# Optimization experiments

Measured on AMD Instinct MI355X. Metric: run time of the kernel, lower is better.

## Reference

```python
import jax, jax.numpy as jnp
import numpy as np

N, E, T = 32768, 262144, 262144
DN, DE = 128, 128
EPS = 1e-5  # torch LayerNorm default eps


def layer_norm(x, g, b):
    m = jnp.mean(x, axis=-1, keepdims=True)
    v = jnp.mean((x - m) ** 2, axis=-1, keepdims=True)
    return (x - m) * jax.lax.rsqrt(v + EPS) * g + b


def setup_inputs() -> dict:
    key = jax.random.key(0)
    ks = jax.random.split(key, 16)
    node_embedding = jax.random.normal(ks[0], (N, DN), dtype=jnp.float32)
    edge_embedding = jax.random.normal(ks[1], (E, DE), dtype=jnp.float32)
    i = jax.random.randint(ks[2], (E,), 0, N)
    j = jax.random.randint(ks[3], (E,), 0, N)
    index_i = jax.random.randint(ks[4], (T,), 0, N)
    index_j = jax.random.randint(ks[5], (T,), 0, N)
    index_k = jax.random.randint(ks[6], (T,), 0, N)
    index_ji = jax.random.randint(ks[7], (T,), 0, E)
    index_kj = jax.random.randint(ks[8], (T,), 0, E)
    d3 = 3 * DN + 2 * DE
    W2 = jax.random.normal(ks[9], (2 * DE, DN), dtype=jnp.float32) / np.sqrt(DN)
    b2 = jnp.zeros((2 * DE,), dtype=jnp.float32)
    W3 = jax.random.normal(ks[10], (2 * DE, d3), dtype=jnp.float32) / np.sqrt(d3)
    b3 = jnp.zeros((2 * DE,), dtype=jnp.float32)
    g_c2 = jnp.ones((2 * DE,), jnp.float32); be_c2 = jnp.zeros((2 * DE,), jnp.float32)
    g_c3 = jnp.ones((2 * DE,), jnp.float32); be_c3 = jnp.zeros((2 * DE,), jnp.float32)
    g_c2_2 = jnp.ones((DE,), jnp.float32); be_c2_2 = jnp.zeros((DE,), jnp.float32)
    g_c3_2 = jnp.ones((DE,), jnp.float32); be_c3_2 = jnp.zeros((DE,), jnp.float32)
    return dict(node_embedding=node_embedding, edge_embedding=edge_embedding,
                i=i, j=j, index_i=index_i, index_j=index_j, index_k=index_k,
                index_ji=index_ji, index_kj=index_kj,
                W2=W2, b2=b2, W3=W3, b3=b3,
                g_c2=g_c2, be_c2=be_c2, g_c3=g_c3, be_c3=be_c3,
                g_c2_2=g_c2_2, be_c2_2=be_c2_2, g_c3_2=g_c3_2, be_c3_2=be_c3_2)


def reference(node_embedding, edge_embedding, i, j, index_i, index_j, index_k,
              index_ji, index_kj, W2, b2, W3, b3,
              g_c2, be_c2, g_c3, be_c3, g_c2_2, be_c2_2, g_c3_2, be_c3_2):
    num_edges = edge_embedding.shape[0]
    # --- c2 branch: per-edge elementwise product of endpoint node embeddings ---
    c2 = node_embedding[i] * node_embedding[j]                      # [E, Dn]
    c2 = layer_norm(c2 @ W2.T + b2, g_c2, be_c2)                    # [E, 2De]
    c2_filter, c2_core = jnp.split(c2, 2, axis=1)
    c2_emb = layer_norm(jax.nn.sigmoid(c2_filter) * jnp.tanh(c2_core), g_c2_2, be_c2_2)
    # --- c3 branch: triplet gather -> linear -> LN -> gate -> scatter-sum ---
    c3 = jnp.concatenate([node_embedding[index_i], node_embedding[index_j],
                          node_embedding[index_k], edge_embedding[index_ji],
                          edge_embedding[index_kj]], axis=1)        # [T, 3Dn+2De]
    c3 = layer_norm(c3 @ W3.T + b3, g_c3, be_c3)                    # [T, 2De]
    c3_filter, c3_core = jnp.split(c3, 2, axis=1)
    msg = jax.nn.sigmoid(c3_filter) * jnp.tanh(c3_core)             # [T, De]
    c3_emb = jax.ops.segment_sum(msg, index_ji, num_segments=num_edges)  # [E, De]
    c3_emb = layer_norm(c3_emb, g_c3_2, be_c3_2)
    return jnp.tanh(edge_embedding + c2_emb + c3_emb)
```

## Files before the change

kernel.cpp:

```cpp
#include <hip/hip_runtime.h>

typedef _Float16 h16;
typedef _Float16 h16x8 __attribute__((ext_vector_type(8)));
typedef float    f32x4 __attribute__((ext_vector_type(4)));

static constexpr int NN  = 32768;
static constexpr int EE  = 262144;
static constexpr int TT  = 262144;
static constexpr int D   = 128;
static constexpr int K3  = 640;
static constexpr int LDA = 72;
#define EPS 1e-5f

__global__ __launch_bounds__(256) void cvt_f32_f16(
    const float* __restrict__ src, h16* __restrict__ dst, int n8)
{
    const int i = blockIdx.x * 256 + threadIdx.x;
    if (i >= n8) return;
    const float4* s = reinterpret_cast<const float4*>(src);
    const float4 a = s[2 * i], b = s[2 * i + 1];
    h16x8 o;
    o[0] = (h16)a.x; o[1] = (h16)a.y; o[2] = (h16)a.z; o[3] = (h16)a.w;
    o[4] = (h16)b.x; o[5] = (h16)b.y; o[6] = (h16)b.z; o[7] = (h16)b.w;
    *reinterpret_cast<h16x8*>(dst + 8 * i) = o;
}

__global__ __launch_bounds__(256, 2) void c3_kernel(
    const h16*  __restrict__ nodeh, const float* __restrict__ edge,
    const int* __restrict__ idx_i, const int* __restrict__ idx_j,
    const int* __restrict__ idx_k, const int* __restrict__ idx_ji,
    const int* __restrict__ idx_kj,
    const h16* __restrict__ W3h, const float* __restrict__ b3,
    const float* __restrict__ g3, const float* __restrict__ be3,
    float* __restrict__ acc3)
{
    __shared__ h16 As[128 * LDA];
    __shared__ h16 Bs[256 * LDA];

    const int tid  = threadIdx.x;
    const int lane = tid & 63;
    const int wave = tid >> 6;
    const int l15  = lane & 15;
    const int quad = lane >> 4;
    const int m0   = blockIdx.x * 128;

    f32x4 acc[2][16];
    #pragma unroll
    for (int mt = 0; mt < 2; ++mt)
        #pragma unroll
        for (int nt = 0; nt < 16; ++nt)
            acc[mt][nt] = (f32x4){0.f, 0.f, 0.f, 0.f};

    const int r = tid >> 1;
    const int h = tid & 1;

    #pragma unroll 1
    for (int c = 0; c < 10; ++c) {
        const int seg  = c >> 1;
        const int half = c & 1;
        const int* idxarr = (seg == 0) ? idx_i : (seg == 1) ? idx_j
                          : (seg == 2) ? idx_k : (seg == 3) ? idx_ji : idx_kj;
        const size_t row = (size_t)idxarr[m0 + r];
        h16x8 av[4];
        if (seg < 3) {
            const h16x8* sp = reinterpret_cast<const h16x8*>(nodeh + row * D + half * 64 + h * 32);
            #pragma unroll
            for (int q = 0; q < 4; ++q) av[q] = sp[q];
        } else {
            const float4* fp = reinterpret_cast<const float4*>(edge + row * D + half * 64 + h * 32);
            #pragma unroll
            for (int q = 0; q < 4; ++q) {
                const float4 u = fp[2 * q], v = fp[2 * q + 1];
                h16x8 t;
                t[0] = (h16)u.x; t[1] = (h16)u.y; t[2] = (h16)u.z; t[3] = (h16)u.w;
                t[4] = (h16)v.x; t[5] = (h16)v.y; t[6] = (h16)v.z; t[7] = (h16)v.w;
                av[q] = t;
            }
        }
        const h16x8* wp = reinterpret_cast<const h16x8*>(W3h + (size_t)tid * K3 + c * 64);
        h16x8 bv[8];
        #pragma unroll
        for (int q = 0; q < 8; ++q) bv[q] = wp[q];

        __syncthreads();
        h16x8* ad = reinterpret_cast<h16x8*>(&As[r * LDA + h * 32]);
        #pragma unroll
        for (int q = 0; q < 4; ++q) ad[q] = av[q];
        h16x8* bd = reinterpret_cast<h16x8*>(&Bs[tid * LDA]);
        #pragma unroll
        for (int q = 0; q < 8; ++q) bd[q] = bv[q];
        __syncthreads();

        #pragma unroll
        for (int kk = 0; kk < 64; kk += 32) {
            h16x8 a0 = *reinterpret_cast<const h16x8*>(&As[(wave*32      + l15) * LDA + kk + quad*8]);
            h16x8 a1 = *reinterpret_cast<const h16x8*>(&As[(wave*32 + 16 + l15) * LDA + kk + quad*8]);
            #pragma unroll
            for (int nt = 0; nt < 16; ++nt) {
                h16x8 b = *reinterpret_cast<const h16x8*>(&Bs[(nt*16 + l15) * LDA + kk + quad*8]);
                acc[0][nt] = __builtin_amdgcn_mfma_f32_16x16x32_f16(a0, b, acc[0][nt], 0, 0, 0);
                acc[1][nt] = __builtin_amdgcn_mfma_f32_16x16x32_f16(a1, b, acc[1][nt], 0, 0, 0);
            }
        }
    }

    float bias[16], gg[16], bb[16];
    #pragma unroll
    for (int nt = 0; nt < 16; ++nt) {
        const int cc = nt * 16 + l15;
        bias[nt] = b3[cc]; gg[nt] = g3[cc]; bb[nt] = be3[cc];
    }
    #pragma unroll
    for (int mt = 0; mt < 2; ++mt) {
        #pragma unroll
        for (int rg = 0; rg < 4; ++rg) {
            float v[16];
            float s = 0.f, s2 = 0.f;
            #pragma unroll
            for (int nt = 0; nt < 16; ++nt) {
                v[nt] = acc[mt][nt][rg] + bias[nt];
                s += v[nt]; s2 += v[nt] * v[nt];
            }
            #pragma unroll
            for (int m = 1; m < 16; m <<= 1) {
                s  += __shfl_xor(s,  m, 64);
                s2 += __shfl_xor(s2, m, 64);
            }
            const float mean = s * (1.f / 256.f);
            const float var  = s2 * (1.f / 256.f) - mean * mean;
            const float inv  = rsqrtf(var + EPS);
            const int rowg   = m0 + wave * 32 + mt * 16 + quad * 4 + rg;
            const size_t e   = (size_t)idx_ji[rowg];
            #pragma unroll
            for (int nt = 0; nt < 8; ++nt) {
                const float f   = (v[nt]     - mean) * inv * gg[nt]     + bb[nt];
                const float co  = (v[nt + 8] - mean) * inv * gg[nt + 8] + bb[nt + 8];
                const float msg = (1.f / (1.f + __expf(-f))) * tanhf(co);
                atomicAdd(&acc3[e * D + nt * 16 + l15], msg);
            }
        }
    }
}

__global__ __launch_bounds__(256, 2) void c2_kernel(
    const h16* __restrict__ nodeh,
    const int* __restrict__ ei, const int* __restrict__ ej,
    const h16* __restrict__ W2h, const float* __restrict__ b2,
    const float* __restrict__ g2, const float* __restrict__ be2,
    const float* __restrict__ g22, const float* __restrict__ be22,
    h16* __restrict__ c2emb)
{
    __shared__ h16 As[128 * LDA];
    __shared__ h16 Bs[256 * LDA];

    const int tid  = threadIdx.x;
    const int lane = tid & 63;
    const int wave = tid >> 6;
    const int l15  = lane & 15;
    const int quad = lane >> 4;
    const int m0   = blockIdx.x * 128;

    f32x4 acc[2][16];
    #pragma unroll
    for (int mt = 0; mt < 2; ++mt)
        #pragma unroll
        for (int nt = 0; nt < 16; ++nt)
            acc[mt][nt] = (f32x4){0.f, 0.f, 0.f, 0.f};

    const int r = tid >> 1;
    const int h = tid & 1;
    const size_t ri = (size_t)ei[m0 + r];
    const size_t rj = (size_t)ej[m0 + r];

    #pragma unroll 1
    for (int c = 0; c < 2; ++c) {
        const h16x8* si = reinterpret_cast<const h16x8*>(nodeh + ri * D + c * 64 + h * 32);
        const h16x8* sj = reinterpret_cast<const h16x8*>(nodeh + rj * D + c * 64 + h * 32);
        h16x8 av[4];
        #pragma unroll
        for (int q = 0; q < 4; ++q) av[q] = si[q] * sj[q];
        const h16x8* wp = reinterpret_cast<const h16x8*>(W2h + (size_t)tid * D + c * 64);
        h16x8 bv[8];
        #pragma unroll
        for (int q = 0; q < 8; ++q) bv[q] = wp[q];

        __syncthreads();
        h16x8* ad = reinterpret_cast<h16x8*>(&As[r * LDA + h * 32]);
        #pragma unroll
        for (int q = 0; q < 4; ++q) ad[q] = av[q];
        h16x8* bd = reinterpret_cast<h16x8*>(&Bs[tid * LDA]);
        #pragma unroll
        for (int q = 0; q < 8; ++q) bd[q] = bv[q];
        __syncthreads();

        #pragma unroll
        for (int kk = 0; kk < 64; kk += 32) {
            h16x8 a0 = *reinterpret_cast<const h16x8*>(&As[(wave*32      + l15) * LDA + kk + quad*8]);
            h16x8 a1 = *reinterpret_cast<const h16x8*>(&As[(wave*32 + 16 + l15) * LDA + kk + quad*8]);
            #pragma unroll
            for (int nt = 0; nt < 16; ++nt) {
                h16x8 b = *reinterpret_cast<const h16x8*>(&Bs[(nt*16 + l15) * LDA + kk + quad*8]);
                acc[0][nt] = __builtin_amdgcn_mfma_f32_16x16x32_f16(a0, b, acc[0][nt], 0, 0, 0);
                acc[1][nt] = __builtin_amdgcn_mfma_f32_16x16x32_f16(a1, b, acc[1][nt], 0, 0, 0);
            }
        }
    }

    float bias[16], gg[16], bb[16];
    #pragma unroll
    for (int nt = 0; nt < 16; ++nt) {
        const int cc = nt * 16 + l15;
        bias[nt] = b2[cc]; gg[nt] = g2[cc]; bb[nt] = be2[cc];
    }
    float g2c[8], b2c[8];
    #pragma unroll
    for (int nt = 0; nt < 8; ++nt) {
        const int cc = nt * 16 + l15;
        g2c[nt] = g22[cc]; b2c[nt] = be22[cc];
    }
    #pragma unroll
    for (int mt = 0; mt < 2; ++mt) {
        #pragma unroll
        for (int rg = 0; rg < 4; ++rg) {
            float v[16];
            float s = 0.f, s2 = 0.f;
            #pragma unroll
            for (int nt = 0; nt < 16; ++nt) {
                v[nt] = acc[mt][nt][rg] + bias[nt];
                s += v[nt]; s2 += v[nt] * v[nt];
            }
            #pragma unroll
            for (int m = 1; m < 16; m <<= 1) {
                s  += __shfl_xor(s,  m, 64);
                s2 += __shfl_xor(s2, m, 64);
            }
            const float mean = s * (1.f / 256.f);
            const float var  = s2 * (1.f / 256.f) - mean * mean;
            const float inv  = rsqrtf(var + EPS);
            float msg[8];
            float t = 0.f, t2 = 0.f;
            #pragma unroll
            for (int nt = 0; nt < 8; ++nt) {
                const float f  = (v[nt]     - mean) * inv * gg[nt]     + bb[nt];
                const float co = (v[nt + 8] - mean) * inv * gg[nt + 8] + bb[nt + 8];
                const float m_ = (1.f / (1.f + __expf(-f))) * tanhf(co);
                msg[nt] = m_; t += m_; t2 += m_ * m_;
            }
            #pragma unroll
            for (int m = 1; m < 16; m <<= 1) {
                t  += __shfl_xor(t,  m, 64);
                t2 += __shfl_xor(t2, m, 64);
            }
            const float mean2 = t * (1.f / 128.f);
            const float var2  = t2 * (1.f / 128.f) - mean2 * mean2;
            const float inv2  = rsqrtf(var2 + EPS);
            const size_t rowg = (size_t)(m0 + wave * 32 + mt * 16 + quad * 4 + rg);
            #pragma unroll
            for (int nt = 0; nt < 8; ++nt) {
                const float o = (msg[nt] - mean2) * inv2 * g2c[nt] + b2c[nt];
                c2emb[rowg * D + nt * 16 + l15] = (h16)o;
            }
        }
    }
}

__global__ __launch_bounds__(256) void final_kernel(
    const float* __restrict__ edge, const h16* __restrict__ c2emb,
    const float* __restrict__ g32, const float* __restrict__ be32,
    float* out)
{
    const int lane = threadIdx.x & 63;
    const int wave = threadIdx.x >> 6;
    const size_t e = (size_t)blockIdx.x * 4 + wave;
    const int c0 = lane * 2;

    const float2 v = *reinterpret_cast<const float2*>(&out[e * D + c0]);
    float s  = v.x + v.y;
    float s2 = v.x * v.x + v.y * v.y;
    #pragma unroll
    for (int m = 1; m < 64; m <<= 1) {
        s  += __shfl_xor(s,  m, 64);
        s2 += __shfl_xor(s2, m, 64);
    }
    const float mean = s * (1.f / 128.f);
    const float var  = s2 * (1.f / 128.f) - mean * mean;
    const float inv  = rsqrtf(var + EPS);
    const float c3a = (v.x - mean) * inv * g32[c0]     + be32[c0];
    const float c3b = (v.y - mean) * inv * g32[c0 + 1] + be32[c0 + 1];

    const float2 ev = *reinterpret_cast<const float2*>(&edge[e * D + c0]);
    const float ca = (float)c2emb[e * D + c0];
    const float cb = (float)c2emb[e * D + c0 + 1];
    float2 o;
    o.x = tanhf(ev.x + ca + c3a);
    o.y = tanhf(ev.y + cb + c3b);
    *reinterpret_cast<float2*>(&out[e * D + c0]) = o;
}

extern "C" void kernel_launch(void* const* d_in, const int* in_sizes, int n_in,
                              void* d_out, int out_size, void* d_ws, size_t ws_size,
                              hipStream_t stream)
{
    const float* node   = (const float*)d_in[0];
    const float* edge   = (const float*)d_in[1];
    const int*   e_i    = (const int*)d_in[2];
    const int*   e_j    = (const int*)d_in[3];
    const int*   idx_i  = (const int*)d_in[4];
    const int*   idx_j  = (const int*)d_in[5];
    const int*   idx_k  = (const int*)d_in[6];
    const int*   idx_ji = (const int*)d_in[7];
    const int*   idx_kj = (const int*)d_in[8];
    const float* W2     = (const float*)d_in[9];
    const float* b2     = (const float*)d_in[10];
    const float* W3     = (const float*)d_in[11];
    const float* b3     = (const float*)d_in[12];
    const float* g_c2   = (const float*)d_in[13];
    const float* be_c2  = (const float*)d_in[14];
    const float* g_c3   = (const float*)d_in[15];
    const float* be_c3  = (const float*)d_in[16];
    const float* g_c22  = (const float*)d_in[17];
    const float* be_c22 = (const float*)d_in[18];
    const float* g_c32  = (const float*)d_in[19];
    const float* be_c32 = (const float*)d_in[20];

    h16* W3h   = (h16*)d_ws;
    h16* W2h   = W3h + 256 * K3;
    h16* nodeh = W2h + 256 * D;
    h16* c2emb = nodeh + (size_t)NN * D;
    float* acc3 = (float*)d_out;
    float* out  = (float*)d_out;

    hipMemsetAsync(d_out, 0, (size_t)EE * D * sizeof(float), stream);
    cvt_f32_f16<<<dim3((256 * K3 / 8 + 255) / 256), dim3(256), 0, stream>>>(W3, W3h, 256 * K3 / 8);
    cvt_f32_f16<<<dim3((256 * D  / 8 + 255) / 256), dim3(256), 0, stream>>>(W2, W2h, 256 * D / 8);
    cvt_f32_f16<<<dim3((NN * D   / 8 + 255) / 256), dim3(256), 0, stream>>>(node, nodeh, NN * D / 8);

    c3_kernel<<<dim3(TT / 128), dim3(256), 0, stream>>>(
        nodeh, edge, idx_i, idx_j, idx_k, idx_ji, idx_kj, W3h, b3, g_c3, be_c3, acc3);
    c2_kernel<<<dim3(EE / 128), dim3(256), 0, stream>>>(
        nodeh, e_i, e_j, W2h, b2, g_c2, be_c2, g_c22, be_c22, c2emb);
    final_kernel<<<dim3(EE / 4), dim3(256), 0, stream>>>(
        edge, c2emb, g_c32, be_c32, out);
}
```

Measured before the change: 699.4 us.

## Double-buffer c3 GEMM with async global-to-LDS loads and fuse final into c2

The c3 kernel now stages A and B tiles through double-buffered LDS using global_load_lds direct DMA with XOR swizzling and K-chunks of 32. Indices are preloaded once, and occupancy is raised to 3 blocks per CU. Edge embeddings are pre-converted to fp16 so they can be DMA'd like node rows. The final LayerNorm/tanh pass is fused into the c2 epilogue, which removes the c2emb intermediate and one kernel launch, at the cost of an extra full edge conversion pass and more register pressure.

```diff
diff --git a/kernel.cpp b/kernel.cpp
--- a/kernel.cpp
+++ b/kernel.cpp
@@ -3,6 +3,7 @@
 typedef _Float16 h16;
 typedef _Float16 h16x8 __attribute__((ext_vector_type(8)));
 typedef float    f32x4 __attribute__((ext_vector_type(4)));
+typedef unsigned long long u64;
 
 static constexpr int NN  = 32768;
 static constexpr int EE  = 262144;
@@ -11,6 +12,12 @@
 static constexpr int K3  = 640;
 static constexpr int LDA = 72;
 #define EPS 1e-5f
+
+__device__ __forceinline__ void async16(const void* g, void* l) {
+    __builtin_amdgcn_global_load_lds(
+        (const __attribute__((address_space(1))) unsigned int*)g,
+        (__attribute__((address_space(3))) unsigned int*)l, 16, 0, 0);
+}
 
 __global__ __launch_bounds__(256) void cvt_f32_f16(
     const float* __restrict__ src, h16* __restrict__ dst, int n8)
@@ -25,8 +32,8 @@
     *reinterpret_cast<h16x8*>(dst + 8 * i) = o;
 }
 
-__global__ __launch_bounds__(256, 2) void c3_kernel(
-    const h16*  __restrict__ nodeh, const float* __restrict__ edge,
+__global__ __launch_bounds__(256, 3) void c3_kernel(
+    const h16* __restrict__ nodeh, const h16* __restrict__ edgeh,
     const int* __restrict__ idx_i, const int* __restrict__ idx_j,
     const int* __restrict__ idx_k, const int* __restrict__ idx_ji,
     const int* __restrict__ idx_kj,
@@ -34,8 +41,8 @@
     const float* __restrict__ g3, const float* __restrict__ be3,
     float* __restrict__ acc3)
 {
-    __shared__ h16 As[128 * LDA];
-    __shared__ h16 Bs[256 * LDA];
+    __shared__ h16 As[2 * 128 * 32];
+    __shared__ h16 Bs[2 * 256 * 32];
 
     const int tid  = threadIdx.x;
     const int lane = tid & 63;
@@ -44,6 +51,16 @@
     const int quad = lane >> 4;
     const int m0   = blockIdx.x * 128;
 
+    const int lr   = lane >> 2;
+    const int gswz = (((lane & 3) ^ ((lane >> 3) & 3)) << 4);
+
+    const int ra0 = m0 + wave * 32 + lr, ra1 = ra0 + 16;
+    const int ix0a = idx_i[ra0],  ix0b = idx_i[ra1];
+    const int ix1a = idx_j[ra0],  ix1b = idx_j[ra1];
+    const int ix2a = idx_k[ra0],  ix2b = idx_k[ra1];
+    const int ix3a = idx_ji[ra0], ix3b = idx_ji[ra1];
+    const int ix4a = idx_kj[ra0], ix4b = idx_kj[ra1];
+
     f32x4 acc[2][16];
     #pragma unroll
     for (int mt = 0; mt < 2; ++mt)
@@ -51,56 +68,51 @@
         for (int nt = 0; nt < 16; ++nt)
             acc[mt][nt] = (f32x4){0.f, 0.f, 0.f, 0.f};
 
-    const int r = tid >> 1;
-    const int h = tid & 1;
+    const char* nb = (const char*)nodeh;
+    const char* eb = (const char*)edgeh;
+    const char* wb = (const char*)W3h;
+    const int browbase = wave * 64 + lr;
+
+    auto dma_chunk = [&](int c) {
+        const int buf = c & 1;
+        h16* Asb = &As[buf * 4096];
+        h16* Bsb = &Bs[buf * 8192];
+        const int seg = c >> 2;
+        const int ia = seg == 0 ? ix0a : seg == 1 ? ix1a : seg == 2 ? ix2a
+                     : seg == 3 ? ix3a : ix4a;
+        const int ib = seg == 0 ? ix0b : seg == 1 ? ix1b : seg == 2 ? ix2b
+                     : seg == 3 ? ix3b : ix4b;
+        const char* src = (seg < 3) ? nb : eb;
+        const int co = (c & 3) * 64;
+        async16(src + (u64)ia * 256 + co + gswz, &Asb[(wave * 32) * 32]);
+        async16(src + (u64)ib * 256 + co + gswz, &Asb[(wave * 32 + 16) * 32]);
+        const int cb = c * 64;
+        #pragma unroll
+        for (int q = 0; q < 4; ++q) {
+            const int roff = (browbase + q * 16) * 1280 + gswz + cb;
+            async16(wb + roff, &Bsb[(wave * 64 + q * 16) * 32]);
+        }
+    };
+
+    dma_chunk(0);
+
+    const int p8    = ((quad ^ ((l15 >> 1) & 3)) << 3);
+    const int abase = (wave * 32 + l15) * 32 + p8;
+    const int bbase = l15 * 32 + p8;
 
     #pragma unroll 1
-    for (int c = 0; c < 10; ++c) {
-        const int seg  = c >> 1;
-        const int half = c & 1;
-        const int* idxarr = (seg == 0) ? idx_i : (seg == 1) ? idx_j
-                          : (seg == 2) ? idx_k : (seg == 3) ? idx_ji : idx_kj;
-        const size_t row = (size_t)idxarr[m0 + r];
-        h16x8 av[4];
-        if (seg < 3) {
-            const h16x8* sp = reinterpret_cast<const h16x8*>(nodeh + row * D + half * 64 + h * 32);
-            #pragma unroll
-            for (int q = 0; q < 4; ++q) av[q] = sp[q];
-        } else {
-            const float4* fp = reinterpret_cast<const float4*>(edge + row * D + half * 64 + h * 32);
-            #pragma unroll
-            for (int q = 0; q < 4; ++q) {
-                const float4 u = fp[2 * q], v = fp[2 * q + 1];
-                h16x8 t;
-                t[0] = (h16)u.x; t[1] = (h16)u.y; t[2] = (h16)u.z; t[3] = (h16)u.w;
-                t[4] = (h16)v.x; t[5] = (h16)v.y; t[6] = (h16)v.z; t[7] = (h16)v.w;
-                av[q] = t;
-            }
-        }
-        const h16x8* wp = reinterpret_cast<const h16x8*>(W3h + (size_t)tid * K3 + c * 64);
-        h16x8 bv[8];
-        #pragma unroll
-        for (int q = 0; q < 8; ++q) bv[q] = wp[q];
-
+    for (int c = 0; c < 20; ++c) {
         __syncthreads();
-        h16x8* ad = reinterpret_cast<h16x8*>(&As[r * LDA + h * 32]);
-        #pragma unroll
-        for (int q = 0; q < 4; ++q) ad[q] = av[q];
-        h16x8* bd = reinterpret_cast<h16x8*>(&Bs[tid * LDA]);
-        #pragma unroll
-        for (int q = 0; q < 8; ++q) bd[q] = bv[q];
-        __syncthreads();
-
-        #pragma unroll
-        for (int kk = 0; kk < 64; kk += 32) {
-            h16x8 a0 = *reinterpret_cast<const h16x8*>(&As[(wave*32      + l15) * LDA + kk + quad*8]);
-            h16x8 a1 = *reinterpret_cast<const h16x8*>(&As[(wave*32 + 16 + l15) * LDA + kk + quad*8]);
-            #pragma unroll
-            for (int nt = 0; nt < 16; ++nt) {
-                h16x8 b = *reinterpret_cast<const h16x8*>(&Bs[(nt*16 + l15) * LDA + kk + quad*8]);
-                acc[0][nt] = __builtin_amdgcn_mfma_f32_16x16x32_f16(a0, b, acc[0][nt], 0, 0, 0);
-                acc[1][nt] = __builtin_amdgcn_mfma_f32_16x16x32_f16(a1, b, acc[1][nt], 0, 0, 0);
-            }
+        if (c + 1 < 20) dma_chunk(c + 1);
+        const h16* Asb = &As[(c & 1) * 4096];
+        const h16* Bsb = &Bs[(c & 1) * 8192];
+        h16x8 a0 = *(const h16x8*)&Asb[abase];
+        h16x8 a1 = *(const h16x8*)&Asb[abase + 512];
+        #pragma unroll
+        for (int nt = 0; nt < 16; ++nt) {
+            h16x8 b = *(const h16x8*)&Bsb[bbase + nt * 512];
+            acc[0][nt] = __builtin_amdgcn_mfma_f32_16x16x32_f16(a0, b, acc[0][nt], 0, 0, 0);
+            acc[1][nt] = __builtin_amdgcn_mfma_f32_16x16x32_f16(a1, b, acc[1][nt], 0, 0, 0);
         }
     }
 
@@ -142,13 +154,14 @@
     }
 }
 
-__global__ __launch_bounds__(256, 2) void c2_kernel(
+__global__ __launch_bounds__(256, 2) void c2final_kernel(
     const h16* __restrict__ nodeh,
     const int* __restrict__ ei, const int* __restrict__ ej,
     const h16* __restrict__ W2h, const float* __restrict__ b2,
     const float* __restrict__ g2, const float* __restrict__ be2,
     const float* __restrict__ g22, const float* __restrict__ be22,
-    h16* __restrict__ c2emb)
+    const float* __restrict__ g32, const float* __restrict__ be32,
+    const float* __restrict__ edge, float* __restrict__ out)
 {
     __shared__ h16 As[128 * LDA];
     __shared__ h16 Bs[256 * LDA];
@@ -212,11 +225,12 @@
         const int cc = nt * 16 + l15;
         bias[nt] = b2[cc]; gg[nt] = g2[cc]; bb[nt] = be2[cc];
     }
-    float g2c[8], b2c[8];
+    float g2c[8], b2c[8], g3c[8], b3c[8];
     #pragma unroll
     for (int nt = 0; nt < 8; ++nt) {
         const int cc = nt * 16 + l15;
         g2c[nt] = g22[cc]; b2c[nt] = be22[cc];
+        g3c[nt] = g32[cc]; b3c[nt] = be32[cc];
     }
     #pragma unroll
     for (int mt = 0; mt < 2; ++mt) {
@@ -254,47 +268,32 @@
             const float mean2 = t * (1.f / 128.f);
             const float var2  = t2 * (1.f / 128.f) - mean2 * mean2;
             const float inv2  = rsqrtf(var2 + EPS);
-            const size_t rowg = (size_t)(m0 + wave * 32 + mt * 16 + quad * 4 + rg);
+
+            const size_t e = (size_t)(m0 + wave * 32 + mt * 16 + quad * 4 + rg);
+            float a3[8];
+            float sa = 0.f, sa2 = 0.f;
             #pragma unroll
             for (int nt = 0; nt < 8; ++nt) {
-                const float o = (msg[nt] - mean2) * inv2 * g2c[nt] + b2c[nt];
-                c2emb[rowg * D + nt * 16 + l15] = (h16)o;
-            }
-        }
-    }
-}
-
-__global__ __launch_bounds__(256) void final_kernel(
-    const float* __restrict__ edge, const h16* __restrict__ c2emb,
-    const float* __restrict__ g32, const float* __restrict__ be32,
-    float* out)
-{
-    const int lane = threadIdx.x & 63;
-    const int wave = threadIdx.x >> 6;
-    const size_t e = (size_t)blockIdx.x * 4 + wave;
-    const int c0 = lane * 2;
-
-    const float2 v = *reinterpret_cast<const float2*>(&out[e * D + c0]);
-    float s  = v.x + v.y;
-    float s2 = v.x * v.x + v.y * v.y;
-    #pragma unroll
-    for (int m = 1; m < 64; m <<= 1) {
-        s  += __shfl_xor(s,  m, 64);
-        s2 += __shfl_xor(s2, m, 64);
-    }
-    const float mean = s * (1.f / 128.f);
-    const float var  = s2 * (1.f / 128.f) - mean * mean;
-    const float inv  = rsqrtf(var + EPS);
-    const float c3a = (v.x - mean) * inv * g32[c0]     + be32[c0];
-    const float c3b = (v.y - mean) * inv * g32[c0 + 1] + be32[c0 + 1];
-
-    const float2 ev = *reinterpret_cast<const float2*>(&edge[e * D + c0]);
-    const float ca = (float)c2emb[e * D + c0];
-    const float cb = (float)c2emb[e * D + c0 + 1];
-    float2 o;
-    o.x = tanhf(ev.x + ca + c3a);
-    o.y = tanhf(ev.y + cb + c3b);
-    *reinterpret_cast<float2*>(&out[e * D + c0]) = o;
+                a3[nt] = out[e * D + nt * 16 + l15];
+                sa += a3[nt]; sa2 += a3[nt] * a3[nt];
+            }
+            #pragma unroll
+            for (int m = 1; m < 16; m <<= 1) {
+                sa  += __shfl_xor(sa,  m, 64);
+                sa2 += __shfl_xor(sa2, m, 64);
+            }
+            const float mean3 = sa * (1.f / 128.f);
+            const float var3  = sa2 * (1.f / 128.f) - mean3 * mean3;
+            const float inv3  = rsqrtf(var3 + EPS);
+            #pragma unroll
+            for (int nt = 0; nt < 8; ++nt) {
+                const float c2v = (msg[nt] - mean2) * inv2 * g2c[nt] + b2c[nt];
+                const float c3v = (a3[nt]  - mean3) * inv3 * g3c[nt] + b3c[nt];
+                const float ev  = edge[e * D + nt * 16 + l15];
+                out[e * D + nt * 16 + l15] = tanhf(ev + c2v + c3v);
+            }
+        }
+    }
 }
 
 extern "C" void kernel_launch(void* const* d_in, const int* in_sizes, int n_in,
@@ -326,7 +325,7 @@
     h16* W3h   = (h16*)d_ws;
     h16* W2h   = W3h + 256 * K3;
     h16* nodeh = W2h + 256 * D;
-    h16* c2emb = nodeh + (size_t)NN * D;
+    h16* edgeh = nodeh + (size_t)NN * D;
     float* acc3 = (float*)d_out;
     float* out  = (float*)d_out;
 
@@ -334,11 +333,10 @@
     cvt_f32_f16<<<dim3((256 * K3 / 8 + 255) / 256), dim3(256), 0, stream>>>(W3, W3h, 256 * K3 / 8);
     cvt_f32_f16<<<dim3((256 * D  / 8 + 255) / 256), dim3(256), 0, stream>>>(W2, W2h, 256 * D / 8);
     cvt_f32_f16<<<dim3((NN * D   / 8 + 255) / 256), dim3(256), 0, stream>>>(node, nodeh, NN * D / 8);
+    cvt_f32_f16<<<dim3(((int)((size_t)EE * D / 8) + 255) / 256), dim3(256), 0, stream>>>(edge, edgeh, (int)((size_t)EE * D / 8));
 
     c3_kernel<<<dim3(TT / 128), dim3(256), 0, stream>>>(
-        nodeh, edge, idx_i, idx_j, idx_k, idx_ji, idx_kj, W3h, b3, g_c3, be_c3, acc3);
-    c2_kernel<<<dim3(EE / 128), dim3(256), 0, stream>>>(
-        nodeh, e_i, e_j, W2h, b2, g_c2, be_c2, g_c22, be_c22, c2emb);
-    final_kernel<<<dim3(EE / 4), dim3(256), 0, stream>>>(
-        edge, c2emb, g_c32, be_c32, out);
-}
+        nodeh, edgeh, idx_i, idx_j, idx_k, idx_ji, idx_kj, W3h, b3, g_c3, be_c3, acc3);
+    c2final_kernel<<<dim3(EE / 128), dim3(256), 0, stream>>>(
+        nodeh, e_i, e_j, W2h, b2, g_c2, be_c2, g_c22, be_c22, g_c32, be_c32, edge, out);
+}
```

Result: slower. 803.0 us (+14.8%).
